# Optimization experiments

Hardware: AMD Instinct MI355X
Metric: run time of the kernel (lower is better)

## Reference

```python
import jax, jax.numpy as jnp
import numpy as np

B, T = 4, 1024
MF, EF, DM, DF, HN, L = 256, 512, 512, 2048, 8, 6
HD = DM // HN  # 64
D = MF + EF // 2  # 512, feature dim of x / mask_in


def prelu(x, a):
    return jnp.where(x >= 0, x, a * x)


def layer_norm(x, g, b, eps=1e-5):
    m = x.mean(-1, keepdims=True)
    v = ((x - m) ** 2).mean(-1, keepdims=True)
    return (x - m) / jnp.sqrt(v + eps) * g + b


def skew_relative(QE):
    # QE: (B, H, N, 2N-1) -> (B, H, N, N) via the pad/reshape/slice skew trick
    b, h, n = QE.shape[0], QE.shape[1], QE.shape[2]
    q = jnp.pad(QE, ((0, 0), (0, 0), (0, 0), (0, 1))).reshape(b, h, -1)
    q = jnp.pad(q, ((0, 0), (0, 0), (0, n - 1))).reshape(b, h, n + 1, 2 * n - 1)
    return q[:, :, :n, -n:]


def setup_inputs() -> dict:
    key = jax.random.key(0)
    ks = iter(jax.random.split(key, 80))
    rn = lambda shape, s: jax.random.normal(next(ks), shape, dtype=jnp.float32) * s
    si = lambda fan: fan ** -0.5
    inp = {}
    inp['x'] = rn((B, T, D), 1.0)
    inp['mask_in'] = (jax.random.uniform(next(ks), (B, T, D)) > 0.2).astype(jnp.float32)
    inp['p_kf'] = rn((B, T, 2), 1.0)
    inp['enc_w1'] = rn((2 * D, DM), si(2 * D)); inp['enc_b1'] = jnp.zeros((DM,)); inp['enc_a1'] = 0.25 * jnp.ones((1,))
    inp['enc_w2'] = rn((DM, DM), si(DM)); inp['enc_b2'] = jnp.zeros((DM,)); inp['enc_a2'] = 0.25 * jnp.ones((1,))
    inp['kf_w1'] = rn((2, DM), si(2)); inp['kf_b1'] = jnp.zeros((DM,)); inp['kf_a'] = 0.25 * jnp.ones((1,))
    inp['kf_w2'] = rn((DM, DM), si(DM)); inp['kf_b2'] = jnp.zeros((DM,))
    inp['rel_w1'] = rn((1, DM), 1.0); inp['rel_b1'] = jnp.zeros((DM,)); inp['rel_a'] = 0.25 * jnp.ones((1,))
    inp['rel_w2'] = rn((DM, HD), si(DM)); inp['rel_b2'] = jnp.zeros((HD,))
    inp['ln_g'] = jnp.ones((DM,)); inp['ln_b'] = jnp.zeros((DM,))
    inp['attn_wq'] = rn((L, DM, DM), si(DM))
    inp['attn_wk'] = rn((L, DM, DM), si(DM))
    inp['attn_wv'] = rn((L, DM, DM), si(DM))
    inp['attn_wo'] = rn((L, DM, DM), si(DM)); inp['attn_wob'] = jnp.zeros((L, DM))
    inp['ffn_w1'] = rn((L, DM, DF), si(DM)); inp['ffn_b1'] = jnp.zeros((L, DF)); inp['ffn_a'] = 0.25 * jnp.ones((L, 1))
    inp['ffn_w2'] = rn((L, DF, DM), si(DF)); inp['ffn_b2'] = jnp.zeros((L, DM))
    inp['dec_w1'] = rn((DM, DM), si(DM)); inp['dec_b1'] = jnp.zeros((DM,)); inp['dec_a'] = 0.25 * jnp.ones((1,))
    inp['dec_w2'] = rn((DM, MF), si(DM)); inp['dec_b2'] = jnp.zeros((MF,))
    return inp


def reference(x, mask_in, p_kf, enc_w1, enc_b1, enc_a1, enc_w2, enc_b2, enc_a2,
              kf_w1, kf_b1, kf_a, kf_w2, kf_b2, rel_w1, rel_b1, rel_a, rel_w2, rel_b2,
              ln_g, ln_b, attn_wq, attn_wk, attn_wv, attn_wo, attn_wob,
              ffn_w1, ffn_b1, ffn_a, ffn_w2, ffn_b2, dec_w1, dec_b1, dec_a, dec_w2, dec_b2):
    b, t, _ = x.shape
    # keyframe positional encoding + context encoder
    pe_kf = prelu(p_kf @ kf_w1 + kf_b1, kf_a) @ kf_w2 + kf_b2
    h = prelu(jnp.concatenate([x, mask_in], -1) @ enc_w1 + enc_b1, enc_a1)
    h = prelu(h @ enc_w2 + enc_b2, enc_a2) + pe_kf
    # relative position embedding table E: (2T-1, HD)
    rel = jnp.arange(-t + 1, t, dtype=jnp.float32)[:, None]
    E = prelu(rel @ rel_w1 + rel_b1, rel_a) @ rel_w2 + rel_b2
    # attention mask from mask_in (broadcast over heads/queries)
    valid = mask_in.sum(-1) > 0
    mask_att = jnp.where(valid, 0.0, -1e9)[:, None, None, :]  # (B,1,1,T)
    scale = HD ** -0.5
    nl = attn_wq.shape[0]
    for i in range(nl):
        hn = layer_norm(h, ln_g, ln_b)
        Q = (hn @ attn_wq[i]).reshape(b, t, HN, HD).transpose(0, 2, 1, 3)
        K = (hn @ attn_wk[i]).reshape(b, t, HN, HD).transpose(0, 2, 1, 3)
        V = (hn @ attn_wv[i]).reshape(b, t, HN, HD).transpose(0, 2, 1, 3)
        att = jnp.einsum('bhqd,bhkd->bhqk', Q, K)
        att = att + skew_relative(jnp.einsum('bhqd,rd->bhqr', Q, E))
        att = jax.nn.softmax(att * scale + mask_att, axis=-1)
        o = jnp.einsum('bhqk,bhkd->bhqd', att, V).transpose(0, 2, 1, 3).reshape(b, t, HN * HD)
        h = h + o @ attn_wo[i] + attn_wob[i]
        hn = layer_norm(h, ln_g, ln_b)
        h = h + prelu(hn @ ffn_w1[i] + ffn_b1[i], ffn_a[i]) @ ffn_w2[i] + ffn_b2[i]
    return prelu(h @ dec_w1 + dec_b1, dec_a) @ dec_w2 + dec_b2
```

## Files before the change

kernel.cpp:

```cpp
#include <hip/hip_runtime.h>
#include <cstddef>

#define BB 4
#define TT 1024
#define DMODEL 512
#define DFF 2048
#define NHEAD 8
#define HDIM 64
#define NTOK (BB*TT)
#define NLAYER 6
#define MFOUT 256
#define LDS_STRIDE 72
#define SPLITK 4

typedef __attribute__((ext_vector_type(8))) _Float16 f16x8;
typedef __attribute__((ext_vector_type(8))) short bf16x8;
typedef __attribute__((ext_vector_type(4))) float f32x4;
#define MFMAH(a,b,c) __builtin_amdgcn_mfma_f32_16x16x32_f16(a,b,c,0,0,0)
#define MFMAB(a,b,c) __builtin_amdgcn_mfma_f32_16x16x32_bf16(a,b,c,0,0,0)

union F16U { _Float16 h; unsigned short u; };

__device__ __forceinline__ unsigned f2bf(float f) {
    union { float f; unsigned u; } v; v.f = f;
    return (v.u + 0x7FFFu + ((v.u >> 16) & 1u)) >> 16;
}
__device__ __forceinline__ float bf2f(unsigned h) {
    union { unsigned u; float f; } v; v.u = h << 16;
    return v.f;
}
__device__ __forceinline__ unsigned short f16u(float v) {
    F16U t; t.h = (_Float16)v; return t.u;
}

#define MODE_F32  0
#define MODE_BF   1
#define MODE_QKV  5

__global__ __launch_bounds__(256)
void wcvt(const float* __restrict__ W, unsigned short* __restrict__ Wh,
          unsigned short* __restrict__ Wl, int N, int K)
{
    __shared__ unsigned short Hs[64][LDS_STRIDE];
    __shared__ unsigned short Ls[64][LDS_STRIDE];
    const int tid = threadIdx.x;
    const int n0 = blockIdx.x * 64, k0 = blockIdx.y * 64;
    #pragma unroll
    for (int i = 0; i < 4; i++) {
        const int idx = tid + i * 256;
        const int r = idx >> 4, c4 = (idx & 15) * 4;
        const float4 v = *(const float4*)&W[(size_t)(k0 + r) * N + n0 + c4];
        const float va[4] = {v.x, v.y, v.z, v.w};
        #pragma unroll
        for (int j = 0; j < 4; j++) {
            const unsigned h = f2bf(va[j]);
            Hs[c4 + j][r] = (unsigned short)h;
            Ls[c4 + j][r] = (unsigned short)f2bf(va[j] - bf2f(h));
        }
    }
    __syncthreads();
    #pragma unroll
    for (int i = 0; i < 2; i++) {
        const int idx = tid + i * 256;
        const int r = idx >> 3, c8 = (idx & 7) * 8;
        *(uint4*)&Wh[(size_t)(n0 + r) * K + k0 + c8] = *(const uint4*)&Hs[r][c8];
        *(uint4*)&Wl[(size_t)(n0 + r) * K + k0 + c8] = *(const uint4*)&Ls[r][c8];
    }
}

__global__ __launch_bounds__(256)
void gemm_l(const unsigned short* __restrict__ Ah, const unsigned short* __restrict__ Al,
            const unsigned short* __restrict__ Wh, const unsigned short* __restrict__ Wl,
            const float* __restrict__ bias, const float* __restrict__ alpha,
            const float* __restrict__ res, float* __restrict__ outf,
            unsigned short* __restrict__ o1, unsigned short* __restrict__ o2,
            unsigned short* __restrict__ o3, unsigned short* __restrict__ o4,
            unsigned short* __restrict__ o5, int N, int K, int mode)
{
    __shared__ __align__(16) unsigned short Ahs[64*LDS_STRIDE];
    __shared__ __align__(16) unsigned short Als[64*LDS_STRIDE];
    __shared__ __align__(16) unsigned short Whs[64*LDS_STRIDE];
    __shared__ __align__(16) unsigned short Wls[64*LDS_STRIDE];
    const int tid = threadIdx.x;
    const int lane = tid & 63, w = tid >> 6;
    const int wm = w >> 1, wn = w & 1;
    const int quad = lane >> 4, c = lane & 15;
    const int m0 = blockIdx.y * 64, n0 = blockIdx.x * 64;
    const int sr = tid >> 2, sc = (tid & 3) * 16;

    f32x4 acc[2][2];
    #pragma unroll
    for (int mi = 0; mi < 2; mi++)
        #pragma unroll
        for (int ni = 0; ni < 2; ni++) { acc[mi][ni][0]=0.f; acc[mi][ni][1]=0.f; acc[mi][ni][2]=0.f; acc[mi][ni][3]=0.f; }

    for (int k0 = 0; k0 < K; k0 += 64) {
        const size_t ga = (size_t)(m0 + sr) * K + k0 + sc;
        const size_t gb = (size_t)(n0 + sr) * K + k0 + sc;
        const int ls = sr * LDS_STRIDE + sc;
        *(uint4*)&Ahs[ls]     = *(const uint4*)&Ah[ga];
        *(uint4*)&Ahs[ls + 8] = *(const uint4*)&Ah[ga + 8];
        *(uint4*)&Als[ls]     = *(const uint4*)&Al[ga];
        *(uint4*)&Als[ls + 8] = *(const uint4*)&Al[ga + 8];
        *(uint4*)&Whs[ls]     = *(const uint4*)&Wh[gb];
        *(uint4*)&Whs[ls + 8] = *(const uint4*)&Wh[gb + 8];
        *(uint4*)&Wls[ls]     = *(const uint4*)&Wl[gb];
        *(uint4*)&Wls[ls + 8] = *(const uint4*)&Wl[gb + 8];
        __syncthreads();
        #pragma unroll
        for (int s = 0; s < 2; s++) {
            const int ao = (wm * 32 + c) * LDS_STRIDE + s * 32 + quad * 8;
            const int bo = (wn * 32 + c) * LDS_STRIDE + s * 32 + quad * 8;
            const bf16x8 ah0 = *(const bf16x8*)&Ahs[ao];
            const bf16x8 ah1 = *(const bf16x8*)&Ahs[ao + 16 * LDS_STRIDE];
            const bf16x8 al0 = *(const bf16x8*)&Als[ao];
            const bf16x8 al1 = *(const bf16x8*)&Als[ao + 16 * LDS_STRIDE];
            const bf16x8 bh0 = *(const bf16x8*)&Whs[bo];
            const bf16x8 bh1 = *(const bf16x8*)&Whs[bo + 16 * LDS_STRIDE];
            const bf16x8 bl0 = *(const bf16x8*)&Wls[bo];
            const bf16x8 bl1 = *(const bf16x8*)&Wls[bo + 16 * LDS_STRIDE];
            acc[0][0] = MFMAB(ah0, bh0, acc[0][0]);
            acc[0][1] = MFMAB(ah0, bh1, acc[0][1]);
            acc[1][0] = MFMAB(ah1, bh0, acc[1][0]);
            acc[1][1] = MFMAB(ah1, bh1, acc[1][1]);
            acc[0][0] = MFMAB(al0, bh0, acc[0][0]);
            acc[0][1] = MFMAB(al0, bh1, acc[0][1]);
            acc[1][0] = MFMAB(al1, bh0, acc[1][0]);
            acc[1][1] = MFMAB(al1, bh1, acc[1][1]);
            acc[0][0] = MFMAB(ah0, bl0, acc[0][0]);
            acc[0][1] = MFMAB(ah0, bl1, acc[0][1]);
            acc[1][0] = MFMAB(ah1, bl0, acc[1][0]);
            acc[1][1] = MFMAB(ah1, bl1, acc[1][1]);
        }
        __syncthreads();
    }
    const float alv = alpha ? alpha[0] : 0.f;
    #pragma unroll
    for (int mi = 0; mi < 2; mi++)
        #pragma unroll
        for (int ni = 0; ni < 2; ni++) {
            const int gn = n0 + wn * 32 + ni * 16 + c;
            const int gmb = m0 + wm * 32 + mi * 16 + quad * 4;
            const float bv = bias ? bias[gn] : 0.f;
            float v4[4];
            #pragma unroll
            for (int r = 0; r < 4; r++) {
                float v = acc[mi][ni][r] + bv;
                if (alpha) v = (v >= 0.f) ? v : alv * v;
                v4[r] = v;
            }
            if (mode == MODE_F32) {
                #pragma unroll
                for (int r = 0; r < 4; r++) {
                    const size_t oix = (size_t)(gmb + r) * N + gn;
                    outf[oix] = v4[r] + (res ? res[oix] : 0.f);
                }
            } else if (mode == MODE_BF) {
                #pragma unroll
                for (int r = 0; r < 4; r++) {
                    const size_t oix = (size_t)(gmb + r) * N + gn;
                    const unsigned h = f2bf(v4[r]);
                    o1[oix] = (unsigned short)h;
                    o2[oix] = (unsigned short)f2bf(v4[r] - bf2f(h));
                }
            } else {
                const int seg = gn >> 9;
                if (seg == 0) {
                    #pragma unroll
                    for (int r = 0; r < 4; r++) {
                        const size_t qix = (size_t)(gmb + r) * 512 + gn;
                        F16U t; t.h = (_Float16)v4[r];
                        o1[qix] = t.u;
                        o2[qix] = f16u((v4[r] - (float)t.h) * 1024.f);
                    }
                } else if (seg == 1) {
                    #pragma unroll
                    for (int r = 0; r < 4; r++)
                        o3[(size_t)(gmb + r) * 512 + (gn - 512)] = f16u(v4[r]);
                } else {
                    const int d512 = gn - 1024;
                    const int bbp = gmb >> 10, t0 = gmb & 1023;
                    const size_t vix = ((size_t)(bbp * 8 + (d512 >> 6)) * 64 + (d512 & 63)) * 1024 + t0;
                    ushort4 hv, lv;
                    unsigned short* hp = (unsigned short*)&hv;
                    unsigned short* lp = (unsigned short*)&lv;
                    #pragma unroll
                    for (int r = 0; r < 4; r++) {
                        F16U t; t.h = (_Float16)v4[r];
                        hp[r] = t.u;
                        lp[r] = f16u(v4[r] - (float)t.h);
                    }
                    *(ushort4*)&o4[vix] = hv;
                    *(ushort4*)&o5[vix] = lv;
                }
            }
        }
}

__global__ __launch_bounds__(64)
void ln_kernel(const float* __restrict__ x, const float* __restrict__ g,
               const float* __restrict__ b, unsigned short* __restrict__ oh,
               unsigned short* __restrict__ ol)
{
    const int token = blockIdx.x;
    const int lane = threadIdx.x;
    const float* row = x + (size_t)token * DMODEL;
    float v[8];
    *(float4*)&v[0] = *(const float4*)&row[lane * 4];
    *(float4*)&v[4] = *(const float4*)&row[256 + lane * 4];
    float s = 0.f, s2 = 0.f;
    #pragma unroll
    for (int i = 0; i < 8; i++) { s += v[i]; s2 += v[i] * v[i]; }
    #pragma unroll
    for (int off = 1; off < 64; off <<= 1) {
        s  += __shfl_xor(s, off);
        s2 += __shfl_xor(s2, off);
    }
    const float mean = s * (1.f / DMODEL);
    const float var  = s2 * (1.f / DMODEL) - mean * mean;
    const float rstd = rsqrtf(var + 1e-5f);
    #pragma unroll
    for (int hh = 0; hh < 2; hh++) {
        const int base = hh * 256 + lane * 4;
        const float4 gv = *(const float4*)&g[base];
        const float4 bv = *(const float4*)&b[base];
        float o[4];
        o[0] = (v[hh*4+0] - mean) * rstd * gv.x + bv.x;
        o[1] = (v[hh*4+1] - mean) * rstd * gv.y + bv.y;
        o[2] = (v[hh*4+2] - mean) * rstd * gv.z + bv.z;
        o[3] = (v[hh*4+3] - mean) * rstd * gv.w + bv.w;
        ushort4 ph, pl;
        unsigned short* php = (unsigned short*)&ph;
        unsigned short* plp = (unsigned short*)&pl;
        #pragma unroll
        for (int j = 0; j < 4; j++) {
            const unsigned hb = f2bf(o[j]);
            php[j] = (unsigned short)hb;
            plp[j] = (unsigned short)f2bf(o[j] - bf2f(hb));
        }
        *(ushort4*)&oh[(size_t)token * DMODEL + base] = ph;
        *(ushort4*)&ol[(size_t)token * DMODEL + base] = pl;
    }
}

__global__ __launch_bounds__(256)
void cvt_pair(const float* __restrict__ x, unsigned short* __restrict__ oh,
              unsigned short* __restrict__ ol)
{
    const int idx = (blockIdx.x * 256 + threadIdx.x) * 4;
    const float4 v = *(const float4*)&x[idx];
    const float va[4] = {v.x, v.y, v.z, v.w};
    ushort4 ph, pl;
    unsigned short* php = (unsigned short*)&ph;
    unsigned short* plp = (unsigned short*)&pl;
    #pragma unroll
    for (int j = 0; j < 4; j++) {
        const unsigned hb = f2bf(va[j]);
        php[j] = (unsigned short)hb;
        plp[j] = (unsigned short)f2bf(va[j] - bf2f(hb));
    }
    *(ushort4*)&oh[idx] = ph;
    *(ushort4*)&ol[idx] = pl;
}

__global__ __launch_bounds__(256)
void cvt_cat(const float* __restrict__ x, const float* __restrict__ mask,
             unsigned short* __restrict__ oh, unsigned short* __restrict__ ol)
{
    const int idx = (blockIdx.x * 256 + threadIdx.x) * 4;
    const int row = idx >> 10, col = idx & 1023;
    const float* src = (col < 512) ? &x[(size_t)row * 512 + col]
                                   : &mask[(size_t)row * 512 + col - 512];
    const float4 v = *(const float4*)src;
    const float va[4] = {v.x, v.y, v.z, v.w};
    ushort4 ph, pl;
    unsigned short* php = (unsigned short*)&ph;
    unsigned short* plp = (unsigned short*)&pl;
    #pragma unroll
    for (int j = 0; j < 4; j++) {
        const unsigned hb = f2bf(va[j]);
        php[j] = (unsigned short)hb;
        plp[j] = (unsigned short)f2bf(va[j] - bf2f(hb));
    }
    *(ushort4*)&oh[idx] = ph;
    *(ushort4*)&ol[idx] = pl;
}

__global__ __launch_bounds__(64)
void mask_kernel(const float* __restrict__ mask_in, float* __restrict__ mk)
{
    const int token = blockIdx.x;
    const int lane = threadIdx.x;
    const float* row = mask_in + (size_t)token * DMODEL;
    const float4 a = *(const float4*)&row[lane * 4];
    const float4 c = *(const float4*)&row[256 + lane * 4];
    float s = a.x + a.y + a.z + a.w + c.x + c.y + c.z + c.w;
    #pragma unroll
    for (int off = 1; off < 64; off <<= 1) s += __shfl_xor(s, off);
    if (lane == 0) mk[token] = (s > 0.f) ? 0.f : -1e9f;
}

__global__ __launch_bounds__(64)
void e_kernel(const float* __restrict__ w1, const float* __restrict__ b1,
              const float* __restrict__ a1, const float* __restrict__ w2,
              const float* __restrict__ b2,
              unsigned short* __restrict__ Ehi, unsigned short* __restrict__ Elo)
{
    __shared__ float t1[DMODEL];
    const int r = blockIdx.x;
    const int rr = (r > 2046) ? 2046 : r;
    const int lane = threadIdx.x;
    const float rel = (float)rr - 1023.f;
    const float al = a1[0];
    for (int j = lane; j < DMODEL; j += 64) {
        float v = rel * w1[j] + b1[j];
        t1[j] = (v >= 0.f) ? v : al * v;
    }
    __syncthreads();
    float acc = b2[lane];
    for (int j = 0; j < DMODEL; j++)
        acc = fmaf(t1[j], w2[j * HDIM + lane], acc);
    const int g = r >> 4, s = lane >> 5;
    const int l = (((lane >> 3) & 3) << 4) | (r & 15);
    const int j = lane & 7;
    const size_t adr = ((size_t)(g * 2 + s) * 64 + l) * 8 + j;
    F16U t; t.h = (_Float16)acc;
    Ehi[adr] = t.u;
    Elo[adr] = f16u(acc - (float)t.h);
}

__global__ __launch_bounds__(256)
void kf1_kernel(const float* __restrict__ p, const float* __restrict__ w1,
                const float* __restrict__ b1, const float* __restrict__ a1,
                unsigned short* __restrict__ oh, unsigned short* __restrict__ ol)
{
    const int idx = blockIdx.x * 256 + threadIdx.x;
    const int m = idx >> 9, n = idx & 511;
    float v = fmaf(p[m*2], w1[n], fmaf(p[m*2+1], w1[DMODEL + n], b1[n]));
    v = (v >= 0.f) ? v : a1[0] * v;
    const unsigned hb = f2bf(v);
    oh[idx] = (unsigned short)hb;
    ol[idx] = (unsigned short)f2bf(v - bf2f(hb));
}

__global__ __launch_bounds__(512, 2)
void attn_mfma(const _Float16* __restrict__ qhg, const _Float16* __restrict__ qmg,
               const _Float16* __restrict__ kg, const _Float16* __restrict__ vth,
               const _Float16* __restrict__ vtl, const _Float16* __restrict__ Ehi,
               const _Float16* __restrict__ Elo, const float* __restrict__ mk,
               float* __restrict__ Opart, float* __restrict__ Mpart,
               float* __restrict__ Lpart)
{
    __shared__ __align__(16) _Float16 Ks [64*LDS_STRIDE];
    __shared__ __align__(16) _Float16 Vhs[64*LDS_STRIDE];
    __shared__ __align__(16) _Float16 Vls[64*LDS_STRIDE];
    __shared__ __align__(16) _Float16 Phs[128*LDS_STRIDE];
    __shared__ __align__(16) _Float16 Pls[128*LDS_STRIDE];

    const int tid = threadIdx.x;
    const int lane = tid & 63;
    const int w = tid >> 6;
    const int quad = lane >> 4;
    const int c = lane & 15;
    const int q0 = (blockIdx.x >> 2) * 128;
    const int split = blockIdx.x & 3;
    const int hh = blockIdx.y;
    const int bb = blockIdx.z;
    const size_t base = (size_t)bb * TT * DMODEL + (size_t)hh * HDIM;
    const size_t vbase = (size_t)(bb * NHEAD + hh) * HDIM * TT;
    const float* mkp = mk + bb * TT;
    const int srow = tid >> 3;
    const int scol = (tid & 7) * 8;

    f16x8 qh[2], qm[2];
    {
        const size_t qrow = base + (size_t)(q0 + 16 * w + c) * DMODEL;
        #pragma unroll
        for (int s = 0; s < 2; s++) {
            qh[s] = *(const f16x8*)&qhg[qrow + s * 32 + quad * 8];
            qm[s] = *(const f16x8*)&qmg[qrow + s * 32 + quad * 8];
        }
    }

    f32x4 O[4];
    #pragma unroll
    for (int dt = 0; dt < 4; dt++) { O[dt][0]=0.f; O[dt][1]=0.f; O[dt][2]=0.f; O[dt][3]=0.f; }
    float mrun[4] = {-1e30f, -1e30f, -1e30f, -1e30f};
    float lrun[4] = {0.f, 0.f, 0.f, 0.f};
    const int Jb = 48 - 16 * w;

    const int ktlo = split * (16 / SPLITK);
    f16x8 sk, svh, svl;
    {
        const int k0 = ktlo * 64;
        sk  = *(const f16x8*)&kg [base + (size_t)(k0 + srow) * DMODEL + scol];
        svh = *(const f16x8*)&vth[vbase + (size_t)srow * TT + k0 + scol];
        svl = *(const f16x8*)&vtl[vbase + (size_t)srow * TT + k0 + scol];
    }
    for (int kt = ktlo; kt < ktlo + (16 / SPLITK); kt++) {
        const int k0 = kt * 64;
        const int rbase = k0 - q0 + 960;

        *(f16x8*)&Ks [srow * LDS_STRIDE + scol] = sk;
        *(f16x8*)&Vhs[srow * LDS_STRIDE + scol] = svh;
        *(f16x8*)&Vls[srow * LDS_STRIDE + scol] = svl;
        __syncthreads();
        {
            const int kn = (kt + 1 < 16) ? (kt + 1) : kt;
            const int k0n = kn * 64;
            sk  = *(const f16x8*)&kg [base + (size_t)(k0n + srow) * DMODEL + scol];
            svh = *(const f16x8*)&vth[vbase + (size_t)srow * TT + k0n + scol];
            svl = *(const f16x8*)&vtl[vbase + (size_t)srow * TT + k0n + scol];
        }

        f32x4 S[4];
        #pragma unroll
        for (int t = 0; t < 4; t++) { S[t][0]=0.f; S[t][1]=0.f; S[t][2]=0.f; S[t][3]=0.f; }
        #pragma unroll
        for (int t = 0; t < 4; t++) {
            const int ko = (16 * t + c) * LDS_STRIDE + quad * 8;
            #pragma unroll
            for (int s = 0; s < 2; s++) {
                const f16x8 kf = *(const f16x8*)&Ks[ko + s * 32];
                S[t] = MFMAH(qh[s], kf, S[t]);
            }
        }
        float bp[4][5];
        #pragma unroll
        for (int ch = 0; ch < 2; ch++) {
            const int u0 = ch * 3;
            const int nu = ch ? 2 : 3;
            f32x4 R[3], R2[3];
            #pragma unroll
            for (int v = 0; v < 3; v++) {
                if (v >= nu) continue;
                R[v][0]=0.f; R[v][1]=0.f; R[v][2]=0.f; R[v][3]=0.f;
                R2[v][0]=0.f; R2[v][1]=0.f; R2[v][2]=0.f; R2[v][3]=0.f;
            }
            #pragma unroll
            for (int v = 0; v < 3; v++) {
                if (v >= nu) continue;
                const int g = (rbase + Jb + 16 * (u0 + v)) >> 4;
                const size_t eb0 = ((size_t)(g * 2 + 0) * 64 + lane) * 8;
                const size_t eb1 = ((size_t)(g * 2 + 1) * 64 + lane) * 8;
                const f16x8 eh0 = *(const f16x8*)&Ehi[eb0];
                const f16x8 eh1 = *(const f16x8*)&Ehi[eb1];
                const f16x8 el0 = *(const f16x8*)&Elo[eb0];
                const f16x8 el1 = *(const f16x8*)&Elo[eb1];
                R[v]  = MFMAH(qh[0], eh0, R[v]);
                R[v]  = MFMAH(qh[1], eh1, R[v]);
                R[v]  = MFMAH(qh[0], el0, R[v]);
                R[v]  = MFMAH(qh[1], el1, R[v]);
                R2[v] = MFMAH(qm[0], eh0, R2[v]);
                R2[v] = MFMAH(qm[1], eh1, R2[v]);
            }
            #pragma unroll
            for (int v = 0; v < 3; v++) {
                if (v >= nu) continue;
                #pragma unroll
                for (int r = 0; r < 4; r++) {
                    const float rv = fmaf(R2[v][r], 9.765625e-4f, R[v][r]);
                    const int q = quad * 4 + r;
                    const int srcl = (quad << 4) | ((c - q + 15) & 15);
                    bp[r][u0 + v] = __int_as_float(__builtin_amdgcn_ds_bpermute(srcl << 2, __float_as_int(rv)));
                }
            }
        }
        float mkv[4];
        #pragma unroll
        for (int t = 0; t < 4; t++) mkv[t] = mkp[k0 + 16*t + c];
        float tmax[4] = {-3e38f, -3e38f, -3e38f, -3e38f};
        #pragma unroll
        for (int t = 0; t < 4; t++)
            #pragma unroll
            for (int r = 0; r < 4; r++) {
                const int q = quad*4 + r;
                const int jj = 16*t + c - q + 15;
                const float rv = ((jj >> 4) == t) ? bp[r][t] : bp[r][t+1];
                const float v = (S[t][r] + rv) * 0.125f + mkv[t];
                S[t][r] = v;
                tmax[r] = fmaxf(tmax[r], v);
            }
        #pragma unroll
        for (int r = 0; r < 4; r++) {
            tmax[r] = fmaxf(tmax[r], __shfl_xor(tmax[r], 1));
            tmax[r] = fmaxf(tmax[r], __shfl_xor(tmax[r], 2));
            tmax[r] = fmaxf(tmax[r], __shfl_xor(tmax[r], 4));
            tmax[r] = fmaxf(tmax[r], __shfl_xor(tmax[r], 8));
        }
        float corr[4];
        #pragma unroll
        for (int r = 0; r < 4; r++) {
            const float mn = fmaxf(mrun[r], tmax[r]);
            corr[r] = __expf(mrun[r] - mn);
            mrun[r] = mn;
            lrun[r] *= corr[r];
        }
        #pragma unroll
        for (int dt = 0; dt < 4; dt++)
            #pragma unroll
            for (int r = 0; r < 4; r++) O[dt][r] *= corr[r];
        float psum[4] = {0.f, 0.f, 0.f, 0.f};
        #pragma unroll
        for (int t = 0; t < 4; t++)
            #pragma unroll
            for (int r = 0; r < 4; r++) {
                const float p = __expf(S[t][r] - mrun[r]);
                psum[r] += p;
                const _Float16 hp = (_Float16)p;
                Phs[(w*16 + quad*4 + r)*LDS_STRIDE + 16*t + c] = hp;
                Pls[(w*16 + quad*4 + r)*LDS_STRIDE + 16*t + c] = (_Float16)(p - (float)hp);
            }
        #pragma unroll
        for (int r = 0; r < 4; r++) {
            psum[r] += __shfl_xor(psum[r], 1);
            psum[r] += __shfl_xor(psum[r], 2);
            psum[r] += __shfl_xor(psum[r], 4);
            psum[r] += __shfl_xor(psum[r], 8);
            lrun[r] += psum[r];
        }
        f16x8 pfh[2], pfl[2];
        #pragma unroll
        for (int s = 0; s < 2; s++) {
            pfh[s] = *(const f16x8*)&Phs[(w*16 + c)*LDS_STRIDE + s*32 + quad*8];
            pfl[s] = *(const f16x8*)&Pls[(w*16 + c)*LDS_STRIDE + s*32 + quad*8];
        }
        #pragma unroll
        for (int dt = 0; dt < 4; dt++) {
            const int vo = (16 * dt + c) * LDS_STRIDE + quad * 8;
            #pragma unroll
            for (int s = 0; s < 2; s++) {
                const f16x8 vhf = *(const f16x8*)&Vhs[vo + s * 32];
                const f16x8 vlf = *(const f16x8*)&Vls[vo + s * 32];
                O[dt] = MFMAH(pfh[s], vhf, O[dt]);
                O[dt] = MFMAH(pfl[s], vhf, O[dt]);
                O[dt] = MFMAH(pfh[s], vlf, O[dt]);
            }
        }
        __syncthreads();
    }
    const size_t obase = (size_t)((split * BB + bb) * NHEAD + hh) * TT + q0 + 16 * w;
    #pragma unroll
    for (int r = 0; r < 4; r++) {
        if (c == 0) {
            Mpart[obase + quad * 4 + r] = mrun[r];
            Lpart[obase + quad * 4 + r] = lrun[r];
        }
    }
    #pragma unroll
    for (int dt = 0; dt < 4; dt++)
        #pragma unroll
        for (int r = 0; r < 4; r++)
            Opart[(obase + quad * 4 + r) * HDIM + 16 * dt + c] = O[dt][r];
}

__global__ __launch_bounds__(256)
void attn_combine(const float* __restrict__ Opart, const float* __restrict__ Mpart,
                  const float* __restrict__ Lpart,
                  unsigned short* __restrict__ obh, unsigned short* __restrict__ obl)
{
    const int tid = threadIdx.x;
    const int row = blockIdx.x * 16 + (tid >> 4);
    const int d0 = (tid & 15) * 4;
    const int SR = BB * NHEAD * TT;
    float mv[SPLITK];
    float m = -3e38f;
    #pragma unroll
    for (int i = 0; i < SPLITK; i++) { mv[i] = Mpart[i * SR + row]; m = fmaxf(m, mv[i]); }
    float wv[SPLITK];
    float l = 0.f;
    #pragma unroll
    for (int i = 0; i < SPLITK; i++) {
        wv[i] = __expf(mv[i] - m);
        l += wv[i] * Lpart[i * SR + row];
    }
    const float inv = 1.f / l;
    float o[4] = {0.f, 0.f, 0.f, 0.f};
    #pragma unroll
    for (int i = 0; i < SPLITK; i++) {
        const float4 v = *(const float4*)&Opart[((size_t)i * SR + row) * HDIM + d0];
        o[0] = fmaf(wv[i], v.x, o[0]);
        o[1] = fmaf(wv[i], v.y, o[1]);
        o[2] = fmaf(wv[i], v.z, o[2]);
        o[3] = fmaf(wv[i], v.w, o[3]);
    }
    const int q = row & (TT - 1), bh = row >> 10;
    const size_t oix = ((size_t)((bh >> 3) * TT + q)) * DMODEL + (size_t)(bh & 7) * HDIM + d0;
    ushort4 ph, pl;
    unsigned short* php = (unsigned short*)&ph;
    unsigned short* plp = (unsigned short*)&pl;
    #pragma unroll
    for (int j = 0; j < 4; j++) {
        const float v = o[j] * inv;
        const unsigned hb = f2bf(v);
        php[j] = (unsigned short)hb;
        plp[j] = (unsigned short)f2bf(v - bf2f(hb));
    }
    *(ushort4*)&obh[oix] = ph;
    *(ushort4*)&obl[oix] = pl;
}

extern "C" void kernel_launch(void* const* d_in, const int* in_sizes, int n_in,
                              void* d_out, int out_size, void* d_ws, size_t ws_size,
                              hipStream_t stream)
{
    const float* x       = (const float*)d_in[0];
    const float* mask_in = (const float*)d_in[1];
    const float* p_kf    = (const float*)d_in[2];
    const float* enc_w1  = (const float*)d_in[3];
    const float* enc_b1  = (const float*)d_in[4];
    const float* enc_a1  = (const float*)d_in[5];
    const float* enc_w2  = (const float*)d_in[6];
    const float* enc_b2  = (const float*)d_in[7];
    const float* enc_a2  = (const float*)d_in[8];
    const float* kf_w1   = (const float*)d_in[9];
    const float* kf_b1   = (const float*)d_in[10];
    const float* kf_a    = (const float*)d_in[11];
    const float* kf_w2   = (const float*)d_in[12];
    const float* kf_b2   = (const float*)d_in[13];
    const float* rel_w1  = (const float*)d_in[14];
    const float* rel_b1  = (const float*)d_in[15];
    const float* rel_a   = (const float*)d_in[16];
    const float* rel_w2  = (const float*)d_in[17];
    const float* rel_b2  = (const float*)d_in[18];
    const float* ln_g    = (const float*)d_in[19];
    const float* ln_b    = (const float*)d_in[20];
    const float* wq      = (const float*)d_in[21];
    const float* wk      = (const float*)d_in[22];
    const float* wv      = (const float*)d_in[23];
    const float* wo      = (const float*)d_in[24];
    const float* wob     = (const float*)d_in[25];
    const float* fw1     = (const float*)d_in[26];
    const float* fb1     = (const float*)d_in[27];
    const float* fa      = (const float*)d_in[28];
    const float* fw2     = (const float*)d_in[29];
    const float* fb2     = (const float*)d_in[30];
    const float* dw1     = (const float*)d_in[31];
    const float* db1     = (const float*)d_in[32];
    const float* da      = (const float*)d_in[33];
    const float* dw2     = (const float*)d_in[34];
    const float* db2     = (const float*)d_in[35];
    float* out = (float*)d_out;

    char* p = (char*)d_ws;
    const size_t SZ_TD  = (size_t)NTOK * DMODEL;
    float* h = (float*)p;                 p += SZ_TD * 4;
    unsigned short* hnh = (unsigned short*)p; p += SZ_TD * 2;
    unsigned short* hnl = (unsigned short*)p; p += SZ_TD * 2;
    unsigned short* qhg = (unsigned short*)p; p += SZ_TD * 2;
    unsigned short* qmg = (unsigned short*)p; p += SZ_TD * 2;
    unsigned short* kg  = (unsigned short*)p; p += SZ_TD * 2;
    unsigned short* vhg = (unsigned short*)p; p += SZ_TD * 2;
    unsigned short* vlg = (unsigned short*)p; p += SZ_TD * 2;
    unsigned short* obh = (unsigned short*)p; p += SZ_TD * 2;
    unsigned short* obl = (unsigned short*)p; p += SZ_TD * 2;
    unsigned short* midh = (unsigned short*)p; p += (size_t)NTOK * DFF * 2;
    unsigned short* midl = (unsigned short*)p; p += (size_t)NTOK * DFF * 2;
    unsigned short* Ehi = (unsigned short*)p; p += (size_t)2048 * HDIM * 2;
    unsigned short* Elo = (unsigned short*)p; p += (size_t)2048 * HDIM * 2;
    float* mk = (float*)p;                p += (size_t)NTOK * 4;
    unsigned short* qkvh = (unsigned short*)p; p += (size_t)1536 * 512 * 2;
    unsigned short* qkvl = (unsigned short*)p; p += (size_t)1536 * 512 * 2;
    unsigned short* woh  = (unsigned short*)p; p += (size_t)512 * 512 * 2;
    unsigned short* wol  = (unsigned short*)p; p += (size_t)512 * 512 * 2;
    unsigned short* f1h  = (unsigned short*)p; p += (size_t)2048 * 512 * 2;
    unsigned short* f1l  = (unsigned short*)p; p += (size_t)2048 * 512 * 2;
    unsigned short* f2h  = (unsigned short*)p; p += (size_t)512 * 2048 * 2;
    unsigned short* f2l  = (unsigned short*)p; p += (size_t)512 * 2048 * 2;
    float* pe = (float*)obh;
    float* Opart = (float*)midh;
    float* Mpart = (float*)hnh;
    float* Lpart = Mpart + (size_t)SPLITK * BB * NHEAD * TT;

    const dim3 blk256(256), blk64(64), blk512(512);
    const dim3 gN512(8, 64);
    const dim3 gQKV(24, 64);
    const dim3 gFFN1(32, 64);
    const dim3 gN256(4, 64);
    #define NP nullptr

    e_kernel<<<dim3(2048), blk64, 0, stream>>>(rel_w1, rel_b1, rel_a, rel_w2, rel_b2, Ehi, Elo);
    mask_kernel<<<dim3(NTOK), blk64, 0, stream>>>(mask_in, mk);
    wcvt<<<dim3(8, 8), blk256, 0, stream>>>(kf_w2, woh, wol, 512, 512);
    wcvt<<<dim3(8, 16), blk256, 0, stream>>>(enc_w1, f1h, f1l, 512, 1024);
    wcvt<<<dim3(8, 8), blk256, 0, stream>>>(enc_w2, qkvh, qkvl, 512, 512);
    kf1_kernel<<<dim3(NTOK*DMODEL/256), blk256, 0, stream>>>(p_kf, kf_w1, kf_b1, kf_a, qhg, qmg);
    gemm_l<<<gN512, blk256, 0, stream>>>(qhg, qmg, woh, wol, kf_b2, NP, NP, pe,
                                         NP, NP, NP, NP, NP, DMODEL, DMODEL, MODE_F32);
    cvt_cat<<<dim3(NTOK*1024/1024), blk256, 0, stream>>>(x, mask_in, midh, midl);
    gemm_l<<<gN512, blk256, 0, stream>>>(midh, midl, f1h, f1l, enc_b1, enc_a1, NP, NP,
                                         hnh, hnl, NP, NP, NP, DMODEL, 2*DMODEL, MODE_BF);
    gemm_l<<<gN512, blk256, 0, stream>>>(hnh, hnl, qkvh, qkvl, enc_b2, enc_a2, pe, h,
                                         NP, NP, NP, NP, NP, DMODEL, DMODEL, MODE_F32);

    for (int i = 0; i < NLAYER; i++) {
        const size_t wofs = (size_t)i * DMODEL * DMODEL;
        wcvt<<<dim3(8, 8), blk256, 0, stream>>>(wq + wofs, qkvh, qkvl, 512, 512);
        wcvt<<<dim3(8, 8), blk256, 0, stream>>>(wk + wofs, qkvh + 512*512, qkvl + 512*512, 512, 512);
        wcvt<<<dim3(8, 8), blk256, 0, stream>>>(wv + wofs, qkvh + 1024*512, qkvl + 1024*512, 512, 512);
        wcvt<<<dim3(8, 8), blk256, 0, stream>>>(wo + wofs, woh, wol, 512, 512);
        wcvt<<<dim3(32, 8), blk256, 0, stream>>>(fw1 + (size_t)i*DMODEL*DFF, f1h, f1l, 2048, 512);
        wcvt<<<dim3(8, 32), blk256, 0, stream>>>(fw2 + (size_t)i*DFF*DMODEL, f2h, f2l, 512, 2048);

        ln_kernel<<<dim3(NTOK), blk64, 0, stream>>>(h, ln_g, ln_b, hnh, hnl);
        gemm_l<<<gQKV, blk256, 0, stream>>>(hnh, hnl, qkvh, qkvl, NP, NP, NP, NP,
                                            qhg, qmg, kg, vhg, vlg, 1536, DMODEL, MODE_QKV);
        attn_mfma<<<dim3((TT/128)*SPLITK, NHEAD, BB), blk512, 0, stream>>>(
            (const _Float16*)qhg, (const _Float16*)qmg, (const _Float16*)kg,
            (const _Float16*)vhg, (const _Float16*)vlg,
            (const _Float16*)Ehi, (const _Float16*)Elo, mk, Opart, Mpart, Lpart);
        attn_combine<<<dim3(BB*NHEAD*TT/16), blk256, 0, stream>>>(Opart, Mpart, Lpart, obh, obl);
        gemm_l<<<gN512, blk256, 0, stream>>>(obh, obl, woh, wol, wob + (size_t)i*DMODEL,
                                             NP, h, h, NP, NP, NP, NP, NP, DMODEL, DMODEL, MODE_F32);
        ln_kernel<<<dim3(NTOK), blk64, 0, stream>>>(h, ln_g, ln_b, hnh, hnl);
        gemm_l<<<gFFN1, blk256, 0, stream>>>(hnh, hnl, f1h, f1l, fb1 + (size_t)i*DFF, fa + i,
                                             NP, NP, midh, midl, NP, NP, NP, DFF, DMODEL, MODE_BF);
        gemm_l<<<gN512, blk256, 0, stream>>>(midh, midl, f2h, f2l, fb2 + (size_t)i*DMODEL,
                                             NP, h, h, NP, NP, NP, NP, NP, DMODEL, DFF, MODE_F32);
    }
    wcvt<<<dim3(8, 8), blk256, 0, stream>>>(dw1, woh, wol, 512, 512);
    wcvt<<<dim3(4, 8), blk256, 0, stream>>>(dw2, f2h, f2l, 256, 512);
    cvt_pair<<<dim3(SZ_TD/1024), blk256, 0, stream>>>(h, hnh, hnl);
    gemm_l<<<gN512, blk256, 0, stream>>>(hnh, hnl, woh, wol, db1, da, NP, NP,
                                         midh, midl, NP, NP, NP, DMODEL, DMODEL, MODE_BF);
    gemm_l<<<gN256, blk256, 0, stream>>>(midh, midl, f2h, f2l, db2, NP, NP, out,
                                         NP, NP, NP, NP, NP, MFOUT, DMODEL, MODE_F32);
    #undef NP
}
```

Measured before the change: 1.779 ms.

## Add 128x128-tile split-bf16 GEMM kernel and use it for most projections

Introduces gemm_l2, a 128x128 output tile GEMM where each wave computes a 64x64 subtile with 4x4 MFMA accumulators, replacing the 64x64-tile gemm_l for the encoder, QKV, output projection, FFN and decoder GEMMs. Larger tiles raise data reuse from LDS and cut global loads per flop, and the shared epilogue is factored into a helper. The cost is about 72KB of LDS per block, higher register pressure from 16 accumulators, and fewer blocks per grid (128 for N=512), which may underfill the GPU's compute units.

```diff
diff --git a/kernel.cpp b/kernel.cpp
--- a/kernel.cpp
+++ b/kernel.cpp
@@ -65,6 +65,68 @@
         const int r = idx >> 3, c8 = (idx & 7) * 8;
         *(uint4*)&Wh[(size_t)(n0 + r) * K + k0 + c8] = *(const uint4*)&Hs[r][c8];
         *(uint4*)&Wl[(size_t)(n0 + r) * K + k0 + c8] = *(const uint4*)&Ls[r][c8];
+    }
+}
+
+__device__ __forceinline__ void gemm_epilogue(
+    int mode, int gmb, int gn, int N, const float* bias, const float* alpha,
+    float alv, const f32x4& a, const float* __restrict__ res, float* __restrict__ outf,
+    unsigned short* __restrict__ o1, unsigned short* __restrict__ o2,
+    unsigned short* __restrict__ o3, unsigned short* __restrict__ o4,
+    unsigned short* __restrict__ o5)
+{
+    const float bv = bias ? bias[gn] : 0.f;
+    float v4[4];
+    #pragma unroll
+    for (int r = 0; r < 4; r++) {
+        float v = a[r] + bv;
+        if (alpha) v = (v >= 0.f) ? v : alv * v;
+        v4[r] = v;
+    }
+    if (mode == MODE_F32) {
+        #pragma unroll
+        for (int r = 0; r < 4; r++) {
+            const size_t oix = (size_t)(gmb + r) * N + gn;
+            outf[oix] = v4[r] + (res ? res[oix] : 0.f);
+        }
+    } else if (mode == MODE_BF) {
+        #pragma unroll
+        for (int r = 0; r < 4; r++) {
+            const size_t oix = (size_t)(gmb + r) * N + gn;
+            const unsigned h = f2bf(v4[r]);
+            o1[oix] = (unsigned short)h;
+            o2[oix] = (unsigned short)f2bf(v4[r] - bf2f(h));
+        }
+    } else {
+        const int seg = gn >> 9;
+        if (seg == 0) {
+            #pragma unroll
+            for (int r = 0; r < 4; r++) {
+                const size_t qix = (size_t)(gmb + r) * 512 + gn;
+                F16U t; t.h = (_Float16)v4[r];
+                o1[qix] = t.u;
+                o2[qix] = f16u((v4[r] - (float)t.h) * 1024.f);
+            }
+        } else if (seg == 1) {
+            #pragma unroll
+            for (int r = 0; r < 4; r++)
+                o3[(size_t)(gmb + r) * 512 + (gn - 512)] = f16u(v4[r]);
+        } else {
+            const int d512 = gn - 1024;
+            const int bbp = gmb >> 10, t0 = gmb & 1023;
+            const size_t vix = ((size_t)(bbp * 8 + (d512 >> 6)) * 64 + (d512 & 63)) * 1024 + t0;
+            ushort4 hv, lv;
+            unsigned short* hp = (unsigned short*)&hv;
+            unsigned short* lp = (unsigned short*)&lv;
+            #pragma unroll
+            for (int r = 0; r < 4; r++) {
+                F16U t; t.h = (_Float16)v4[r];
+                hp[r] = t.u;
+                lp[r] = f16u(v4[r] - (float)t.h);
+            }
+            *(ushort4*)&o4[vix] = hv;
+            *(ushort4*)&o5[vix] = lv;
+        }
     }
 }
 
@@ -141,59 +203,81 @@
         for (int ni = 0; ni < 2; ni++) {
             const int gn = n0 + wn * 32 + ni * 16 + c;
             const int gmb = m0 + wm * 32 + mi * 16 + quad * 4;
-            const float bv = bias ? bias[gn] : 0.f;
-            float v4[4];
-            #pragma unroll
-            for (int r = 0; r < 4; r++) {
-                float v = acc[mi][ni][r] + bv;
-                if (alpha) v = (v >= 0.f) ? v : alv * v;
-                v4[r] = v;
-            }
-            if (mode == MODE_F32) {
+            gemm_epilogue(mode, gmb, gn, N, bias, alpha, alv, acc[mi][ni],
+                          res, outf, o1, o2, o3, o4, o5);
+        }
+}
+
+__global__ __launch_bounds__(256, 2)
+void gemm_l2(const unsigned short* __restrict__ Ah, const unsigned short* __restrict__ Al,
+             const unsigned short* __restrict__ Wh, const unsigned short* __restrict__ Wl,
+             const float* __restrict__ bias, const float* __restrict__ alpha,
+             const float* __restrict__ res, float* __restrict__ outf,
+             unsigned short* __restrict__ o1, unsigned short* __restrict__ o2,
+             unsigned short* __restrict__ o3, unsigned short* __restrict__ o4,
+             unsigned short* __restrict__ o5, int N, int K, int mode)
+{
+    __shared__ __align__(16) unsigned short Ahs[128*LDS_STRIDE];
+    __shared__ __align__(16) unsigned short Als[128*LDS_STRIDE];
+    __shared__ __align__(16) unsigned short Whs[128*LDS_STRIDE];
+    __shared__ __align__(16) unsigned short Wls[128*LDS_STRIDE];
+    const int tid = threadIdx.x;
+    const int lane = tid & 63, w = tid >> 6;
+    const int wm = w >> 1, wn = w & 1;
+    const int quad = lane >> 4, c = lane & 15;
+    const int m0 = blockIdx.y * 128, n0 = blockIdx.x * 128;
+    const int sr = tid >> 1, sc = (tid & 1) * 32;
+
+    f32x4 acc[4][4];
+    #pragma unroll
+    for (int mi = 0; mi < 4; mi++)
+        #pragma unroll
+        for (int ni = 0; ni < 4; ni++) { acc[mi][ni][0]=0.f; acc[mi][ni][1]=0.f; acc[mi][ni][2]=0.f; acc[mi][ni][3]=0.f; }
+
+    for (int k0 = 0; k0 < K; k0 += 64) {
+        const size_t ga = (size_t)(m0 + sr) * K + k0 + sc;
+        const size_t gb = (size_t)(n0 + sr) * K + k0 + sc;
+        const int ls = sr * LDS_STRIDE + sc;
+        #pragma unroll
+        for (int j = 0; j < 4; j++) {
+            *(uint4*)&Ahs[ls + 8*j] = *(const uint4*)&Ah[ga + 8*j];
+            *(uint4*)&Als[ls + 8*j] = *(const uint4*)&Al[ga + 8*j];
+            *(uint4*)&Whs[ls + 8*j] = *(const uint4*)&Wh[gb + 8*j];
+            *(uint4*)&Wls[ls + 8*j] = *(const uint4*)&Wl[gb + 8*j];
+        }
+        __syncthreads();
+        #pragma unroll
+        for (int s = 0; s < 2; s++) {
+            bf16x8 ah[4], al[4], bh[4], bl[4];
+            #pragma unroll
+            for (int i = 0; i < 4; i++) {
+                const int ao = (wm * 64 + i * 16 + c) * LDS_STRIDE + s * 32 + quad * 8;
+                const int bo = (wn * 64 + i * 16 + c) * LDS_STRIDE + s * 32 + quad * 8;
+                ah[i] = *(const bf16x8*)&Ahs[ao];
+                al[i] = *(const bf16x8*)&Als[ao];
+                bh[i] = *(const bf16x8*)&Whs[bo];
+                bl[i] = *(const bf16x8*)&Wls[bo];
+            }
+            #pragma unroll
+            for (int mi = 0; mi < 4; mi++)
                 #pragma unroll
-                for (int r = 0; r < 4; r++) {
-                    const size_t oix = (size_t)(gmb + r) * N + gn;
-                    outf[oix] = v4[r] + (res ? res[oix] : 0.f);
+                for (int ni = 0; ni < 4; ni++) {
+                    acc[mi][ni] = MFMAB(ah[mi], bh[ni], acc[mi][ni]);
+                    acc[mi][ni] = MFMAB(al[mi], bh[ni], acc[mi][ni]);
+                    acc[mi][ni] = MFMAB(ah[mi], bl[ni], acc[mi][ni]);
                 }
-            } else if (mode == MODE_BF) {
-                #pragma unroll
-                for (int r = 0; r < 4; r++) {
-                    const size_t oix = (size_t)(gmb + r) * N + gn;
-                    const unsigned h = f2bf(v4[r]);
-                    o1[oix] = (unsigned short)h;
-                    o2[oix] = (unsigned short)f2bf(v4[r] - bf2f(h));
-                }
-            } else {
-                const int seg = gn >> 9;
-                if (seg == 0) {
-                    #pragma unroll
-                    for (int r = 0; r < 4; r++) {
-                        const size_t qix = (size_t)(gmb + r) * 512 + gn;
-                        F16U t; t.h = (_Float16)v4[r];
-                        o1[qix] = t.u;
-                        o2[qix] = f16u((v4[r] - (float)t.h) * 1024.f);
-                    }
-                } else if (seg == 1) {
-                    #pragma unroll
-                    for (int r = 0; r < 4; r++)
-                        o3[(size_t)(gmb + r) * 512 + (gn - 512)] = f16u(v4[r]);
-                } else {
-                    const int d512 = gn - 1024;
-                    const int bbp = gmb >> 10, t0 = gmb & 1023;
-                    const size_t vix = ((size_t)(bbp * 8 + (d512 >> 6)) * 64 + (d512 & 63)) * 1024 + t0;
-                    ushort4 hv, lv;
-                    unsigned short* hp = (unsigned short*)&hv;
-                    unsigned short* lp = (unsigned short*)&lv;
-                    #pragma unroll
-                    for (int r = 0; r < 4; r++) {
-                        F16U t; t.h = (_Float16)v4[r];
-                        hp[r] = t.u;
-                        lp[r] = f16u(v4[r] - (float)t.h);
-                    }
-                    *(ushort4*)&o4[vix] = hv;
-                    *(ushort4*)&o5[vix] = lv;
-                }
-            }
+        }
+        __syncthreads();
+    }
+    const float alv = alpha ? alpha[0] : 0.f;
+    #pragma unroll
+    for (int mi = 0; mi < 4; mi++)
+        #pragma unroll
+        for (int ni = 0; ni < 4; ni++) {
+            const int gn = n0 + wn * 64 + ni * 16 + c;
+            const int gmb = m0 + wm * 64 + mi * 16 + quad * 4;
+            gemm_epilogue(mode, gmb, gn, N, bias, alpha, alv, acc[mi][ni],
+                          res, outf, o1, o2, o3, o4, o5);
         }
 }
 
@@ -673,9 +757,9 @@
     float* Lpart = Mpart + (size_t)SPLITK * BB * NHEAD * TT;
 
     const dim3 blk256(256), blk64(64), blk512(512);
-    const dim3 gN512(8, 64);
-    const dim3 gQKV(24, 64);
-    const dim3 gFFN1(32, 64);
+    const dim3 gB512(4, 32);
+    const dim3 gBQKV(12, 32);
+    const dim3 gBFFN1(16, 32);
     const dim3 gN256(4, 64);
     #define NP nullptr
 
@@ -685,13 +769,13 @@
     wcvt<<<dim3(8, 16), blk256, 0, stream>>>(enc_w1, f1h, f1l, 512, 1024);
     wcvt<<<dim3(8, 8), blk256, 0, stream>>>(enc_w2, qkvh, qkvl, 512, 512);
     kf1_kernel<<<dim3(NTOK*DMODEL/256), blk256, 0, stream>>>(p_kf, kf_w1, kf_b1, kf_a, qhg, qmg);
-    gemm_l<<<gN512, blk256, 0, stream>>>(qhg, qmg, woh, wol, kf_b2, NP, NP, pe,
-                                         NP, NP, NP, NP, NP, DMODEL, DMODEL, MODE_F32);
+    gemm_l2<<<gB512, blk256, 0, stream>>>(qhg, qmg, woh, wol, kf_b2, NP, NP, pe,
+                                          NP, NP, NP, NP, NP, DMODEL, DMODEL, MODE_F32);
     cvt_cat<<<dim3(NTOK*1024/1024), blk256, 0, stream>>>(x, mask_in, midh, midl);
-    gemm_l<<<gN512, blk256, 0, stream>>>(midh, midl, f1h, f1l, enc_b1, enc_a1, NP, NP,
-                                         hnh, hnl, NP, NP, NP, DMODEL, 2*DMODEL, MODE_BF);
-    gemm_l<<<gN512, blk256, 0, stream>>>(hnh, hnl, qkvh, qkvl, enc_b2, enc_a2, pe, h,
-                                         NP, NP, NP, NP, NP, DMODEL, DMODEL, MODE_F32);
+    gemm_l2<<<gB512, blk256, 0, stream>>>(midh, midl, f1h, f1l, enc_b1, enc_a1, NP, NP,
+                                          hnh, hnl, NP, NP, NP, DMODEL, 2*DMODEL, MODE_BF);
+    gemm_l2<<<gB512, blk256, 0, stream>>>(hnh, hnl, qkvh, qkvl, enc_b2, enc_a2, pe, h,
+                                          NP, NP, NP, NP, NP, DMODEL, DMODEL, MODE_F32);
 
     for (int i = 0; i < NLAYER; i++) {
         const size_t wofs = (size_t)i * DMODEL * DMODEL;
@@ -703,26 +787,26 @@
         wcvt<<<dim3(8, 32), blk256, 0, stream>>>(fw2 + (size_t)i*DFF*DMODEL, f2h, f2l, 512, 2048);
 
         ln_kernel<<<dim3(NTOK), blk64, 0, stream>>>(h, ln_g, ln_b, hnh, hnl);
-        gemm_l<<<gQKV, blk256, 0, stream>>>(hnh, hnl, qkvh, qkvl, NP, NP, NP, NP,
-                                            qhg, qmg, kg, vhg, vlg, 1536, DMODEL, MODE_QKV);
+        gemm_l2<<<gBQKV, blk256, 0, stream>>>(hnh, hnl, qkvh, qkvl, NP, NP, NP, NP,
+                                              qhg, qmg, kg, vhg, vlg, 1536, DMODEL, MODE_QKV);
         attn_mfma<<<dim3((TT/128)*SPLITK, NHEAD, BB), blk512, 0, stream>>>(
             (const _Float16*)qhg, (const _Float16*)qmg, (const _Float16*)kg,
             (const _Float16*)vhg, (const _Float16*)vlg,
             (const _Float16*)Ehi, (const _Float16*)Elo, mk, Opart, Mpart, Lpart);
         attn_combine<<<dim3(BB*NHEAD*TT/16), blk256, 0, stream>>>(Opart, Mpart, Lpart, obh, obl);
-        gemm_l<<<gN512, blk256, 0, stream>>>(obh, obl, woh, wol, wob + (size_t)i*DMODEL,
-                                             NP, h, h, NP, NP, NP, NP, NP, DMODEL, DMODEL, MODE_F32);
+        gemm_l2<<<gB512, blk256, 0, stream>>>(obh, obl, woh, wol, wob + (size_t)i*DMODEL,
+                                              NP, h, h, NP, NP, NP, NP, NP, DMODEL, DMODEL, MODE_F32);
         ln_kernel<<<dim3(NTOK), blk64, 0, stream>>>(h, ln_g, ln_b, hnh, hnl);
-        gemm_l<<<gFFN1, blk256, 0, stream>>>(hnh, hnl, f1h, f1l, fb1 + (size_t)i*DFF, fa + i,
-                                             NP, NP, midh, midl, NP, NP, NP, DFF, DMODEL, MODE_BF);
-        gemm_l<<<gN512, blk256, 0, stream>>>(midh, midl, f2h, f2l, fb2 + (size_t)i*DMODEL,
-                                             NP, h, h, NP, NP, NP, NP, NP, DMODEL, DFF, MODE_F32);
+        gemm_l2<<<gBFFN1, blk256, 0, stream>>>(hnh, hnl, f1h, f1l, fb1 + (size_t)i*DFF, fa + i,
+                                               NP, NP, midh, midl, NP, NP, NP, DFF, DMODEL, MODE_BF);
+        gemm_l2<<<gB512, blk256, 0, stream>>>(midh, midl, f2h, f2l, fb2 + (size_t)i*DMODEL,
+                                              NP, h, h, NP, NP, NP, NP, NP, DMODEL, DFF, MODE_F32);
     }
     wcvt<<<dim3(8, 8), blk256, 0, stream>>>(dw1, woh, wol, 512, 512);
     wcvt<<<dim3(4, 8), blk256, 0, stream>>>(dw2, f2h, f2l, 256, 512);
     cvt_pair<<<dim3(SZ_TD/1024), blk256, 0, stream>>>(h, hnh, hnl);
-    gemm_l<<<gN512, blk256, 0, stream>>>(hnh, hnl, woh, wol, db1, da, NP, NP,
-                                         midh, midl, NP, NP, NP, DMODEL, DMODEL, MODE_BF);
+    gemm_l2<<<gB512, blk256, 0, stream>>>(hnh, hnl, woh, wol, db1, da, NP, NP,
+                                          midh, midl, NP, NP, NP, DMODEL, DMODEL, MODE_BF);
     gemm_l<<<gN256, blk256, 0, stream>>>(midh, midl, f2h, f2l, db2, NP, NP, out,
                                          NP, NP, NP, NP, NP, MFOUT, DMODEL, MODE_F32);
     #undef NP
```

Result: slower. 2.368 ms (+33.1%).
